# Kernel optimization log

Hardware: AMD Instinct MI355X
Metric: run time of the kernel (lower is better)

The kernel has to match this reference:

```python
import jax, jax.numpy as jnp
import numpy as np

B, C, L = 16, 256, 2048

def setup_inputs() -> dict:
    key = jax.random.key(0)
    k1, k2, k3, k4 = jax.random.split(key, 4)
    return {
        "proj_query": jax.random.normal(k1, (B, C, L), dtype=jnp.float32),
        "proj_key": jax.random.normal(k2, (B, C, L), dtype=jnp.float32),
        "proj_val": jax.random.normal(k3, (B, C, L), dtype=jnp.float32),
        "padding_mask": jax.random.uniform(k4, (B, 1, L), dtype=jnp.float32),
    }

def reference(proj_query, proj_key, proj_val, padding_mask):
    c = proj_query.shape[1]
    # energy[b,l,m] = sum_c Q[b,c,l] * K[b,c,m]  -> (B, L, L)
    energy = jnp.einsum("bcl,bcm->blm", proj_query, proj_key) / jnp.sqrt(jnp.float32(c))
    # log-additive padding mask (the tril mask in the source is dead code, never applied)
    logits = energy + jnp.log(padding_mask + 1e-9)
    attention = jax.nn.softmax(logits, axis=-1)
    # post-softmax multiplicative mask
    attention = attention * padding_mask
    # out[b,c,l] = sum_m V[b,c,m] * attention[b,l,m]  -> (B, C, L)
    out = jnp.einsum("bcm,blm->bcl", proj_val, attention)
    return out
```

## Files before the change

kernel.cpp:

```cpp
#include <hip/hip_runtime.h>
#include <hip/hip_bf16.h>

#define B_ 16
#define C_ 256
#define L_ 2048
#define MT 32

typedef __attribute__((ext_vector_type(8))) short bf16x8;
typedef __attribute__((ext_vector_type(4))) float f32x4;

#define CEXP 0.09016844005556021f

__device__ __forceinline__ short f2bf_rne(float f) {
    union { float f; unsigned u; } x; x.f = f;
    unsigned r = x.u + 0x7fffu + ((x.u >> 16) & 1u);
    return (short)(r >> 16);
}

__device__ __forceinline__ void gld_lds16(const void* g, void* l) {
    __builtin_amdgcn_global_load_lds(
        (const __attribute__((address_space(1))) void*)g,
        (__attribute__((address_space(3))) void*)l, 16, 0, 0);
}

__global__ __launch_bounds__(256) void prepass_kernel(
        const float* __restrict__ Kin, const float* __restrict__ Vin,
        const float* __restrict__ mask,
        short* __restrict__ Kt, short* __restrict__ Vb) {
    const int bid = blockIdx.x;
    const int t = threadIdx.x;
    if (bid < 512) {
        __shared__ unsigned short tile[64 * 256];
        const int b  = bid >> 5;
        const int l0 = (bid & 31) * 64;
        #pragma unroll
        for (int iter = 0; iter < 16; ++iter) {
            int idx = iter * 256 + t;
            int ci = idx >> 4;
            int lc = (idx & 15) * 4;
            float4 v = *(const float4*)(Kin + ((size_t)(b * C_ + ci)) * L_ + l0 + lc);
            float vv[4] = {v.x, v.y, v.z, v.w};
            #pragma unroll
            for (int j = 0; j < 4; ++j) {
                int l = lc + j;
                tile[l * 256 + (((ci >> 3) ^ (l & 31)) << 3) + (ci & 7)] =
                    (unsigned short)f2bf_rne(vv[j]);
            }
        }
        __syncthreads();
        #pragma unroll
        for (int iter = 0; iter < 8; ++iter) {
            int li = iter * 8 + (t >> 5);
            int ck = t & 31;
            uint4 val = *(const uint4*)(tile + li * 256 + ((ck ^ (li & 31)) << 3));
            *(uint4*)(Kt + ((size_t)(b * L_ + l0 + li)) * C_ + ck * 8) = val;
        }
    } else {
        size_t e = ((size_t)(bid - 512) * 256 + t) * 8;
        int b = (int)(e >> 19);
        int m = (int)(e & (L_ - 1));
        const float4 v0 = *(const float4*)(Vin + e);
        const float4 v1 = *(const float4*)(Vin + e + 4);
        const float* mp = mask + ((size_t)b << 11) + m;
        const float4 m0 = *(const float4*)mp;
        const float4 m1 = *(const float4*)(mp + 4);
        uint4 o;
        o.x = (unsigned)(unsigned short)f2bf_rne(v0.x * m0.x)
            | ((unsigned)(unsigned short)f2bf_rne(v0.y * m0.y) << 16);
        o.y = (unsigned)(unsigned short)f2bf_rne(v0.z * m0.z)
            | ((unsigned)(unsigned short)f2bf_rne(v0.w * m0.w) << 16);
        o.z = (unsigned)(unsigned short)f2bf_rne(v1.x * m1.x)
            | ((unsigned)(unsigned short)f2bf_rne(v1.y * m1.y) << 16);
        o.w = (unsigned)(unsigned short)f2bf_rne(v1.z * m1.z)
            | ((unsigned)(unsigned short)f2bf_rne(v1.w * m1.w) << 16);
        *(uint4*)(Vb + e) = o;
    }
}

__device__ __forceinline__ void stage_K(const short* __restrict__ Ksrc,
                                        short* Ks, int m0, int t) {
    #pragma unroll
    for (int rr = 0; rr < 4; ++rr) {
        int G = rr * 256 + t;
        int m = G >> 5, p = G & 31;
        gld_lds16(Ksrc + ((size_t)(m0 + m) << 8) + ((p ^ m) << 3), Ks + G * 8);
    }
}

__device__ __forceinline__ void load_V(bf16x8 (&vf)[4], const short* __restrict__ Vw, int m0) {
    #pragma unroll
    for (int ct = 0; ct < 4; ++ct)
        vf[ct] = *(const bf16x8*)(Vw + (size_t)(ct * 16) * L_ + m0);
}

#define O_PHASE(PBUF, VF)                                                                  \
  {                                                                                        \
    bf16x8 af[4];                                                                          \
    _Pragma("unroll")                                                                      \
    for (int lt = 0; lt < 4; ++lt)                                                         \
      af[lt] = *(const bf16x8*)((PBUF) + (16 * lt + 4 * (n & 3) + (n >> 2)) * 40 + 8 * q); \
    _Pragma("unroll")                                                                      \
    for (int ct = 0; ct < 4; ++ct)                                                         \
      _Pragma("unroll")                                                                    \
      for (int lt = 0; lt < 4; ++lt)                                                       \
        Oacc[lt][ct] =                                                                     \
            __builtin_amdgcn_mfma_f32_16x16x32_bf16(af[lt], (VF)[ct], Oacc[lt][ct], 0, 0, 0); \
  }

#define S_PHASE(KS, PW0)                                                                   \
  {                                                                                        \
    f32x4 S0 = fzero, S1 = fzero;                                                          \
    const short* Krow = (KS) + (16 * mt + n) * 256;                                        \
    _Pragma("unroll")                                                                      \
    for (int ks = 0; ks < 8; ++ks) {                                                       \
      bf16x8 bf = *(const bf16x8*)(Krow + (((4 * ks + q) ^ (16 * mt + n)) << 3));          \
      S0 = __builtin_amdgcn_mfma_f32_16x16x32_bf16(qf[0][ks], bf, S0, 0, 0, 0);            \
      S1 = __builtin_amdgcn_mfma_f32_16x16x32_bf16(qf[1][ks], bf, S1, 0, 0, 0);            \
    }                                                                                      \
    _Pragma("unroll")                                                                      \
    for (int r = 0; r < 4; ++r) {                                                          \
      float p0 = wv * exp2f(S0[r]);                                                        \
      dn[0][r] += p0;                                                                      \
      (PW0)[(4 * r) * 40] = f2bf_rne(p0);                                                  \
      float p1 = wv * exp2f(S1[r]);                                                        \
      dn[1][r] += p1;                                                                      \
      (PW0)[(16 + 4 * r) * 40] = f2bf_rne(p1);                                             \
    }                                                                                      \
  }

__global__ __launch_bounds__(256, 2) void attn_main(
        const float* __restrict__ Qin,
        const short* __restrict__ Kt,
        const short* __restrict__ Vb,
        const float* __restrict__ mask,
        float* __restrict__ out) {
    __shared__ __align__(16) char smem[43520];
    short* KsB0 = (short*)smem;
    short* KsB1 = (short*)(smem + 16384);
    short* PA   = (short*)(smem + 32768);
    short* PB   = (short*)(smem + 37888);
    float* Dsh  = (float*)(smem + 43008);

    const int t = threadIdx.x;
    const int w = t >> 6, lane = t & 63, q = lane >> 4, n = lane & 15;
    const int g = w & 1, mt = w >> 1;

    const int b  = blockIdx.x & 15;
    const int l0 = (blockIdx.x >> 4) * 64;

    const short* Ksrc = Kt + (size_t)b * (L_ * C_);
    const short* Vsrc = Vb + (size_t)b * (C_ * L_);
    const float* mrow = mask + (size_t)b * L_;
    const short* Vw   = Vsrc + (size_t)(64 * w + n) * L_ + 8 * q;
    short* Pw0A = PA + (32 * g + q) * 40 + 16 * mt + n;
    short* Pw0B = PB + (32 * g + q) * 40 + 16 * mt + n;

    bf16x8 qf[2][8];
    {
        const float* Qb = Qin + (size_t)b * (C_ * L_) + (l0 + 32 * g + n);
        #pragma unroll
        for (int lt = 0; lt < 2; ++lt)
            #pragma unroll
            for (int ks = 0; ks < 8; ++ks) {
                bf16x8 v;
                #pragma unroll
                for (int j = 0; j < 8; ++j) {
                    float f = Qb[(size_t)(32 * ks + 8 * q + j) * L_ + 16 * lt];
                    v[j] = f2bf_rne(f * CEXP);
                }
                qf[lt][ks] = v;
            }
    }

    const f32x4 fzero = {0.f, 0.f, 0.f, 0.f};
    f32x4 Oacc[4][4];
    #pragma unroll
    for (int i = 0; i < 4; ++i)
        #pragma unroll
        for (int j = 0; j < 4; ++j) Oacc[i][j] = fzero;
    float dn[2][4] = {{0.f,0.f,0.f,0.f},{0.f,0.f,0.f,0.f}};

    stage_K(Ksrc, KsB0, 0, t);
    bf16x8 vfA[4], vfB[4];
    load_V(vfA, Vw, 0);
    float wv = mrow[16 * mt + n] + 1e-9f;

    #pragma unroll 1
    for (int it2 = 0; it2 < L_ / MT / 2; ++it2) {
        const int m0a = it2 * (2 * MT);
        const int m0b = m0a + MT;

        __syncthreads();
        if (m0a != 0) O_PHASE(PB, vfB)
        stage_K(Ksrc, KsB1, m0a + MT, t);
        load_V(vfB, Vw, m0a + MT);
        float wvn0 = mrow[m0a + MT + 16 * mt + n] + 1e-9f;
        S_PHASE(KsB0, Pw0A)
        wv = wvn0;

        __syncthreads();
        O_PHASE(PA, vfA)
        float wvn1 = 0.f;
        if (m0b + MT < L_) {
            stage_K(Ksrc, KsB0, m0b + MT, t);
            load_V(vfA, Vw, m0b + MT);
            wvn1 = mrow[m0b + MT + 16 * mt + n] + 1e-9f;
        }
        S_PHASE(KsB1, Pw0B)
        wv = wvn1;
    }

    __syncthreads();
    O_PHASE(PB, vfB)

    #pragma unroll
    for (int d = 1; d < 16; d <<= 1) {
        #pragma unroll
        for (int lt = 0; lt < 2; ++lt)
            #pragma unroll
            for (int r = 0; r < 4; ++r)
                dn[lt][r] += __shfl_xor(dn[lt][r], d, 64);
    }
    if (n == 0) {
        #pragma unroll
        for (int lt = 0; lt < 2; ++lt)
            #pragma unroll
            for (int r = 0; r < 4; ++r)
                Dsh[mt * 64 + 32 * g + 16 * lt + 4 * q + r] = dn[lt][r];
    }
    __syncthreads();

    float rden[4][4];
    #pragma unroll
    for (int lt = 0; lt < 4; ++lt)
        #pragma unroll
        for (int r = 0; r < 4; ++r) {
            int l = 16 * lt + 4 * q + r;
            rden[lt][r] = 1.0f / (Dsh[l] + Dsh[64 + l]);
        }

    float* ob = out + (size_t)b * (C_ * L_) + l0;
    #pragma unroll
    for (int lt = 0; lt < 4; ++lt)
        #pragma unroll
        for (int ct = 0; ct < 4; ++ct) {
            int c = 64 * w + 16 * ct + n;
            float4 val;
            val.x = Oacc[lt][ct][0] * rden[lt][0];
            val.y = Oacc[lt][ct][1] * rden[lt][1];
            val.z = Oacc[lt][ct][2] * rden[lt][2];
            val.w = Oacc[lt][ct][3] * rden[lt][3];
            *(float4*)(ob + (size_t)c * L_ + 16 * lt + 4 * q) = val;
        }
}

extern "C" void kernel_launch(void* const* d_in, const int* in_sizes, int n_in,
                              void* d_out, int out_size, void* d_ws, size_t ws_size,
                              hipStream_t stream) {
    const float* Q    = (const float*)d_in[0];
    const float* K    = (const float*)d_in[1];
    const float* V    = (const float*)d_in[2];
    const float* mask = (const float*)d_in[3];
    float* out = (float*)d_out;

    short* Kt = (short*)d_ws;
    short* Vb = Kt + (size_t)B_ * L_ * C_;

    prepass_kernel<<<4608, 256, 0, stream>>>(K, V, mask, Kt, Vb);
    attn_main<<<512, 256, 0, stream>>>(Q, Kt, Vb, mask, out);
}
```

Baseline: 230.3 us.

## Split attention block work across 8 waves instead of 4

```diff
diff --git a/kernel.cpp b/kernel.cpp
--- a/kernel.cpp
+++ b/kernel.cpp
@@ -80,55 +80,51 @@
 __device__ __forceinline__ void stage_K(const short* __restrict__ Ksrc,
                                         short* Ks, int m0, int t) {
     #pragma unroll
-    for (int rr = 0; rr < 4; ++rr) {
-        int G = rr * 256 + t;
+    for (int rr = 0; rr < 2; ++rr) {
+        int G = rr * 512 + t;
         int m = G >> 5, p = G & 31;
         gld_lds16(Ksrc + ((size_t)(m0 + m) << 8) + ((p ^ m) << 3), Ks + G * 8);
     }
 }
 
-__device__ __forceinline__ void load_V(bf16x8 (&vf)[4], const short* __restrict__ Vw, int m0) {
-    #pragma unroll
-    for (int ct = 0; ct < 4; ++ct)
+__device__ __forceinline__ void load_V(bf16x8 (&vf)[2], const short* __restrict__ Vw, int m0) {
+    #pragma unroll
+    for (int ct = 0; ct < 2; ++ct)
         vf[ct] = *(const bf16x8*)(Vw + (size_t)(ct * 16) * L_ + m0);
 }
 
 #define O_PHASE(PBUF, VF)                                                                  \
   {                                                                                        \
-    bf16x8 af[4];                                                                          \
     _Pragma("unroll")                                                                      \
-    for (int lt = 0; lt < 4; ++lt)                                                         \
-      af[lt] = *(const bf16x8*)((PBUF) + (16 * lt + 4 * (n & 3) + (n >> 2)) * 40 + 8 * q); \
-    _Pragma("unroll")                                                                      \
-    for (int ct = 0; ct < 4; ++ct)                                                         \
+    for (int lt = 0; lt < 4; ++lt) {                                                       \
+      bf16x8 af = *(const bf16x8*)((PBUF) + (16 * lt + 4 * (n & 3) + (n >> 2)) * 40 + 8 * q); \
       _Pragma("unroll")                                                                    \
-      for (int lt = 0; lt < 4; ++lt)                                                       \
+      for (int ct = 0; ct < 2; ++ct)                                                       \
         Oacc[lt][ct] =                                                                     \
-            __builtin_amdgcn_mfma_f32_16x16x32_bf16(af[lt], (VF)[ct], Oacc[lt][ct], 0, 0, 0); \
+            __builtin_amdgcn_mfma_f32_16x16x32_bf16(af, (VF)[ct], Oacc[lt][ct], 0, 0, 0);  \
+    }                                                                                      \
   }
 
 #define S_PHASE(KS, PW0)                                                                   \
   {                                                                                        \
-    f32x4 S0 = fzero, S1 = fzero;                                                          \
+    f32x4 Sa = fzero, Sb = fzero;                                                          \
     const short* Krow = (KS) + (16 * mt + n) * 256;                                        \
     _Pragma("unroll")                                                                      \
-    for (int ks = 0; ks < 8; ++ks) {                                                       \
-      bf16x8 bf = *(const bf16x8*)(Krow + (((4 * ks + q) ^ (16 * mt + n)) << 3));          \
-      S0 = __builtin_amdgcn_mfma_f32_16x16x32_bf16(qf[0][ks], bf, S0, 0, 0, 0);            \
-      S1 = __builtin_amdgcn_mfma_f32_16x16x32_bf16(qf[1][ks], bf, S1, 0, 0, 0);            \
+    for (int ks = 0; ks < 4; ++ks) {                                                       \
+      bf16x8 bfa = *(const bf16x8*)(Krow + (((4 * ks + q) ^ (16 * mt + n)) << 3));         \
+      bf16x8 bfb = *(const bf16x8*)(Krow + (((4 * (ks + 4) + q) ^ (16 * mt + n)) << 3));   \
+      Sa = __builtin_amdgcn_mfma_f32_16x16x32_bf16(qf[ks], bfa, Sa, 0, 0, 0);              \
+      Sb = __builtin_amdgcn_mfma_f32_16x16x32_bf16(qf[ks + 4], bfb, Sb, 0, 0, 0);          \
     }                                                                                      \
     _Pragma("unroll")                                                                      \
     for (int r = 0; r < 4; ++r) {                                                          \
-      float p0 = wv * exp2f(S0[r]);                                                        \
-      dn[0][r] += p0;                                                                      \
+      float p0 = wv * exp2f(Sa[r] + Sb[r]);                                                \
+      dn[r] += p0;                                                                         \
       (PW0)[(4 * r) * 40] = f2bf_rne(p0);                                                  \
-      float p1 = wv * exp2f(S1[r]);                                                        \
-      dn[1][r] += p1;                                                                      \
-      (PW0)[(16 + 4 * r) * 40] = f2bf_rne(p1);                                             \
     }                                                                                      \
   }
 
-__global__ __launch_bounds__(256, 2) void attn_main(
+__global__ __launch_bounds__(512, 4) void attn_main(
         const float* __restrict__ Qin,
         const short* __restrict__ Kt,
         const short* __restrict__ Vb,
@@ -143,7 +139,7 @@
 
     const int t = threadIdx.x;
     const int w = t >> 6, lane = t & 63, q = lane >> 4, n = lane & 15;
-    const int g = w & 1, mt = w >> 1;
+    const int g = w & 3, mt = w >> 2;
 
     const int b  = blockIdx.x & 15;
     const int l0 = (blockIdx.x >> 4) * 64;
@@ -151,37 +147,35 @@
     const short* Ksrc = Kt + (size_t)b * (L_ * C_);
     const short* Vsrc = Vb + (size_t)b * (C_ * L_);
     const float* mrow = mask + (size_t)b * L_;
-    const short* Vw   = Vsrc + (size_t)(64 * w + n) * L_ + 8 * q;
-    short* Pw0A = PA + (32 * g + q) * 40 + 16 * mt + n;
-    short* Pw0B = PB + (32 * g + q) * 40 + 16 * mt + n;
-
-    bf16x8 qf[2][8];
+    const short* Vw   = Vsrc + (size_t)(32 * w + n) * L_ + 8 * q;
+    short* Pw0A = PA + (16 * g + q) * 40 + 16 * mt + n;
+    short* Pw0B = PB + (16 * g + q) * 40 + 16 * mt + n;
+
+    bf16x8 qf[8];
     {
-        const float* Qb = Qin + (size_t)b * (C_ * L_) + (l0 + 32 * g + n);
-        #pragma unroll
-        for (int lt = 0; lt < 2; ++lt)
+        const float* Qb = Qin + (size_t)b * (C_ * L_) + (l0 + 16 * g + n);
+        #pragma unroll
+        for (int ks = 0; ks < 8; ++ks) {
+            bf16x8 v;
             #pragma unroll
-            for (int ks = 0; ks < 8; ++ks) {
-                bf16x8 v;
-                #pragma unroll
-                for (int j = 0; j < 8; ++j) {
-                    float f = Qb[(size_t)(32 * ks + 8 * q + j) * L_ + 16 * lt];
-                    v[j] = f2bf_rne(f * CEXP);
-                }
-                qf[lt][ks] = v;
+            for (int j = 0; j < 8; ++j) {
+                float f = Qb[(size_t)(32 * ks + 8 * q + j) * L_];
+                v[j] = f2bf_rne(f * CEXP);
             }
+            qf[ks] = v;
+        }
     }
 
     const f32x4 fzero = {0.f, 0.f, 0.f, 0.f};
-    f32x4 Oacc[4][4];
+    f32x4 Oacc[4][2];
     #pragma unroll
     for (int i = 0; i < 4; ++i)
         #pragma unroll
-        for (int j = 0; j < 4; ++j) Oacc[i][j] = fzero;
-    float dn[2][4] = {{0.f,0.f,0.f,0.f},{0.f,0.f,0.f,0.f}};
+        for (int j = 0; j < 2; ++j) Oacc[i][j] = fzero;
+    float dn[4] = {0.f, 0.f, 0.f, 0.f};
 
     stage_K(Ksrc, KsB0, 0, t);
-    bf16x8 vfA[4], vfB[4];
+    bf16x8 vfA[2], vfB[2];
     load_V(vfA, Vw, 0);
     float wv = mrow[16 * mt + n] + 1e-9f;
 
@@ -216,17 +210,13 @@
     #pragma unroll
     for (int d = 1; d < 16; d <<= 1) {
         #pragma unroll
-        for (int lt = 0; lt < 2; ++lt)
-            #pragma unroll
-            for (int r = 0; r < 4; ++r)
-                dn[lt][r] += __shfl_xor(dn[lt][r], d, 64);
+        for (int r = 0; r < 4; ++r)
+            dn[r] += __shfl_xor(dn[r], d, 64);
     }
     if (n == 0) {
         #pragma unroll
-        for (int lt = 0; lt < 2; ++lt)
-            #pragma unroll
-            for (int r = 0; r < 4; ++r)
-                Dsh[mt * 64 + 32 * g + 16 * lt + 4 * q + r] = dn[lt][r];
+        for (int r = 0; r < 4; ++r)
+            Dsh[mt * 64 + 16 * g + 4 * q + r] = dn[r];
     }
     __syncthreads();
 
@@ -243,8 +233,8 @@
     #pragma unroll
     for (int lt = 0; lt < 4; ++lt)
         #pragma unroll
-        for (int ct = 0; ct < 4; ++ct) {
-            int c = 64 * w + 16 * ct + n;
+        for (int ct = 0; ct < 2; ++ct) {
+            int c = 32 * w + 16 * ct + n;
             float4 val;
             val.x = Oacc[lt][ct][0] * rden[lt][0];
             val.y = Oacc[lt][ct][1] * rden[lt][1];
@@ -267,5 +257,5 @@
     short* Vb = Kt + (size_t)B_ * L_ * C_;
 
     prepass_kernel<<<4608, 256, 0, stream>>>(K, V, mask, Kt, Vb);
-    attn_main<<<512, 256, 0, stream>>>(Q, Kt, Vb, mask, out);
-}
+    attn_main<<<512, 512, 0, stream>>>(Q, Kt, Vb, mask, out);
+}
```

Result: slower. 236.7 us (+2.8%).
